# Optimization experiments

Hardware: AMD Instinct MI355X
Metric: run time of the kernel (lower is better)

## Reference

```python
import jax, jax.numpy as jnp
import numpy as np

B, T, D = 2, 2048, 1024
H, HD = 16, 64  # num_heads, num_hiddens_per_head


def setup_inputs() -> dict:
    key = jax.random.key(0)
    ks = jax.random.split(key, 6)
    scale = 1.0 / np.sqrt(D)
    inputs_q = jax.random.normal(ks[0], (B, T, D), dtype=jnp.float32)
    inputs_kv = jax.random.normal(ks[1], (B, T, D), dtype=jnp.float32)
    # causal mask, broadcastable to [b, h, t, T]
    mask = jnp.tril(jnp.ones((T, T), dtype=bool))[None, None, :, :]
    Wq = jax.random.normal(ks[2], (D, H * HD), dtype=jnp.float32) * scale
    Wk = jax.random.normal(ks[3], (D, H * HD), dtype=jnp.float32) * scale
    Wv = jax.random.normal(ks[4], (D, H * HD), dtype=jnp.float32) * scale
    Wo = jax.random.normal(ks[5], (H * HD, D), dtype=jnp.float32) * scale
    return {"inputs_q": inputs_q, "inputs_kv": inputs_kv, "mask": mask,
            "Wq": Wq, "Wk": Wk, "Wv": Wv, "Wo": Wo}


def reference(inputs_q, inputs_kv, mask, Wq, Wk, Wv, Wo):
    b, t, _ = inputs_q.shape
    q = (inputs_q @ Wq).reshape(b, -1, H, HD)
    k = (inputs_kv @ Wk).reshape(b, -1, H, HD)
    v = (inputs_kv @ Wv).reshape(b, -1, H, HD)
    scores = jnp.einsum('bthd,bThd->bhtT', q, k) * (1.0 / jnp.sqrt(HD))
    scores = jnp.where(mask, scores, jnp.finfo(jnp.float32).min)
    attn = jax.nn.softmax(scores, axis=-1)
    out = jnp.einsum('bhtT,bThd->bthd', attn, v).reshape(b, t, H * HD)
    return out @ Wo
```

## Files before the change

kernel.cpp:

```cpp
#include <hip/hip_runtime.h>
#include <hip/hip_bf16.h>

#define B_  2
#define T_  2048
#define D_  1024
#define H_  16
#define HD_ 64

typedef __bf16 bf16x8 __attribute__((ext_vector_type(8)));
typedef float  f32x4  __attribute__((ext_vector_type(4)));

#define MFIX 8.0f

__device__ __forceinline__ __bf16 f2b(float f) {
  __hip_bfloat16 h = __float2bfloat16(f);
  return *reinterpret_cast<__bf16*>(&h);
}

__device__ __forceinline__ void gload_lds16(const __bf16* g, __bf16* l) {
  __builtin_amdgcn_global_load_lds((const unsigned int*)g, (unsigned int*)l, 16, 0, 0);
}

__global__ __launch_bounds__(256) void prep_k(const float* __restrict__ Xq,
                                              const float* __restrict__ Xkv,
                                              const float* __restrict__ Wq,
                                              const float* __restrict__ Wk,
                                              const float* __restrict__ Wv,
                                              const float* __restrict__ Wo,
                                              __hip_bfloat16* __restrict__ Xq_b,
                                              __hip_bfloat16* __restrict__ Xkv_b,
                                              __hip_bfloat16* __restrict__ WTall,
                                              __hip_bfloat16* __restrict__ WoT) {
  const int blk = blockIdx.x;
  if (blk < 8192) {
    const float* x = (blk < 4096) ? Xq : Xkv;
    __hip_bfloat16* y = (blk < 4096) ? Xq_b : Xkv_b;
    const size_t i = ((size_t)(blk & 4095) * 256 + threadIdx.x) * 4;
    f32x4 v = *(const f32x4*)(x + i);
    union { ushort4 u; __hip_bfloat16 h[4]; } o;
#pragma unroll
    for (int j = 0; j < 4; ++j) o.h[j] = __float2bfloat16(v[j]);
    *(ushort4*)(y + i) = o.u;
    return;
  }
  __shared__ float tile[64][65];
  const int wid  = (blk - 8192) >> 8;
  const int tid_ = (blk - 8192) & 255;
  const float* in = (wid == 0) ? Wq : (wid == 1) ? Wk : (wid == 2) ? Wv : Wo;
  __hip_bfloat16* out = (wid == 3) ? WoT : (WTall + (size_t)wid * 1024 * D_);
  const int bx = (tid_ & 15) * 64, by = (tid_ >> 4) * 64;
  const int tx = threadIdx.x & 63, ty = threadIdx.x >> 6;
#pragma unroll
  for (int i = ty; i < 64; i += 4)
    tile[i][tx] = in[(size_t)(by + i) * D_ + bx + tx];
  __syncthreads();
#pragma unroll
  for (int i = ty; i < 64; i += 4)
    out[(size_t)(bx + i) * D_ + by + tx] = __float2bfloat16(tile[tx][i]);
}

__global__ __launch_bounds__(256) void gemm_qkv_k(const __bf16* __restrict__ Aq,
                                                  const __bf16* __restrict__ Akv,
                                                  const __bf16* __restrict__ WTall,
                                                  __hip_bfloat16* __restrict__ Qd,
                                                  __hip_bfloat16* __restrict__ Kd,
                                                  __hip_bfloat16* __restrict__ Vd) {
  __shared__ __align__(16) __bf16 Al[128 * 32];
  __shared__ __align__(16) __bf16 Bl[128 * 32];
  __shared__ __align__(16) __bf16 Tr[64][136];

  const int bm = blockIdx.x * 128;
  const int bn = blockIdx.y * 128;
  const int w  = bn >> 10;
  const __bf16* A = (w == 0) ? Aq : Akv;

  const int wave = threadIdx.x >> 6, lane = threadIdx.x & 63;
  const int wm = (wave >> 1) * 64, wn = (wave & 1) * 64;
  const int lo = lane & 15, qh = lane >> 4;

  const int srow = threadIdx.x >> 2;
  const int skc  = (threadIdx.x & 3) * 8;
  const __bf16* Ag0 = A      + (size_t)(bm + srow) * D_ + skc;
  const __bf16* Bg0 = WTall  + (size_t)(bn + srow) * D_ + skc;
  __bf16* Al0 = Al + threadIdx.x * 8;
  __bf16* Bl0 = Bl + threadIdx.x * 8;

  f32x4 acc[4][4] = {};

  for (int k0 = 0; k0 < D_; k0 += 32) {
    __syncthreads();
    gload_lds16(Ag0 + k0,           Al0);
    gload_lds16(Ag0 + 64 * D_ + k0, Al0 + 64 * 32);
    gload_lds16(Bg0 + k0,           Bl0);
    gload_lds16(Bg0 + 64 * D_ + k0, Bl0 + 64 * 32);
    __syncthreads();

    bf16x8 af[4], bfr[4];
#pragma unroll
    for (int mt = 0; mt < 4; ++mt)
      af[mt] = *(const bf16x8*)(Al + (wm + mt * 16 + lo) * 32 + qh * 8);
#pragma unroll
    for (int nt = 0; nt < 4; ++nt)
      bfr[nt] = *(const bf16x8*)(Bl + (wn + nt * 16 + lo) * 32 + qh * 8);
#pragma unroll
    for (int mt = 0; mt < 4; ++mt)
#pragma unroll
      for (int nt = 0; nt < 4; ++nt)
        acc[mt][nt] = __builtin_amdgcn_mfma_f32_16x16x32_bf16(af[mt], bfr[nt], acc[mt][nt], 0, 0, 0);
  }

  if (w == 2) {
    const int bV  = bm >> 11;
    const int tV0 = bm & (T_ - 1);
#pragma unroll
    for (int ph = 0; ph < 2; ++ph) {
      __syncthreads();
      if ((wn >> 6) == ph) {
#pragma unroll
        for (int mt = 0; mt < 4; ++mt)
#pragma unroll
          for (int nt = 0; nt < 4; ++nt)
#pragma unroll
            for (int r = 0; r < 4; ++r)
              Tr[nt * 16 + lo][wm + mt * 16 + 4 * qh + r] = f2b(acc[mt][nt][r]);
      }
      __syncthreads();
      const int hcol = ((bn & 1023) >> 6) + ph;
      const int row  = threadIdx.x >> 2;
      const int tc   = (threadIdx.x & 3) * 32;
      __hip_bfloat16* dst = Vd + (((size_t)(bV * H_ + hcol) * HD_ + row) * T_) + tV0 + tc;
#pragma unroll
      for (int j = 0; j < 32; j += 8)
        *(bf16x8*)(__bf16*)(dst + j) = *(const bf16x8*)&Tr[row][tc + j];
    }
  } else {
    __hip_bfloat16* dst = (w == 0) ? Qd : Kd;
    const float scale = (w == 0) ? 0.125f : 1.0f;
    const int col0 = (bn + wn) & 1023;
#pragma unroll
    for (int mt = 0; mt < 4; ++mt)
#pragma unroll
      for (int nt = 0; nt < 4; ++nt)
#pragma unroll
        for (int r = 0; r < 4; ++r) {
          const int m = bm + wm + mt * 16 + 4 * qh + r;
          const int n = col0 + nt * 16 + lo;
          const int b = m >> 11, t = m & (T_ - 1);
          const int h = n >> 6,  d = n & 63;
          dst[(((size_t)(b * H_ + h) * T_ + t) << 6) + d] =
              __float2bfloat16(acc[mt][nt][r] * scale);
        }
  }
}

__global__ __launch_bounds__(256) void gemm_out_k(const __bf16* __restrict__ A,
                                                  const __bf16* __restrict__ Bt,
                                                  float* __restrict__ C) {
  __shared__ __align__(16) __bf16 Al[128 * 32];
  __shared__ __align__(16) __bf16 Bl[64 * 32];

  const int bm = blockIdx.x * 128;
  const int bn = blockIdx.y * 64;
  const int wave = threadIdx.x >> 6, lane = threadIdx.x & 63;
  const int wm = (wave >> 1) * 64, wn = (wave & 1) * 32;
  const int lo = lane & 15, qh = lane >> 4;

  const int srow = threadIdx.x >> 2;
  const int skc  = (threadIdx.x & 3) * 8;
  const __bf16* Ag0 = A  + (size_t)(bm + srow) * D_ + skc;
  const __bf16* Bg0 = Bt + (size_t)(bn + srow) * D_ + skc;
  __bf16* Al0 = Al + threadIdx.x * 8;
  __bf16* Bl0 = Bl + threadIdx.x * 8;

  f32x4 acc[4][2] = {};

  for (int k0 = 0; k0 < D_; k0 += 32) {
    __syncthreads();
    gload_lds16(Ag0 + k0,           Al0);
    gload_lds16(Ag0 + 64 * D_ + k0, Al0 + 64 * 32);
    gload_lds16(Bg0 + k0,           Bl0);
    __syncthreads();

    bf16x8 af[4], bfr[2];
#pragma unroll
    for (int mt = 0; mt < 4; ++mt)
      af[mt] = *(const bf16x8*)(Al + (wm + mt * 16 + lo) * 32 + qh * 8);
#pragma unroll
    for (int nt = 0; nt < 2; ++nt)
      bfr[nt] = *(const bf16x8*)(Bl + (wn + nt * 16 + lo) * 32 + qh * 8);
#pragma unroll
    for (int mt = 0; mt < 4; ++mt)
#pragma unroll
      for (int nt = 0; nt < 2; ++nt)
        acc[mt][nt] = __builtin_amdgcn_mfma_f32_16x16x32_bf16(af[mt], bfr[nt], acc[mt][nt], 0, 0, 0);
  }

#pragma unroll
  for (int mt = 0; mt < 4; ++mt)
#pragma unroll
    for (int nt = 0; nt < 2; ++nt)
#pragma unroll
      for (int r = 0; r < 4; ++r) {
        const int m = bm + wm + mt * 16 + 4 * qh + r;
        const int n = bn + wn + nt * 16 + lo;
        C[(size_t)m * D_ + n] = acc[mt][nt][r];
      }
}

__global__ __launch_bounds__(256) void attn_slice_k(const __hip_bfloat16* __restrict__ Q,
                                                    const __hip_bfloat16* __restrict__ K,
                                                    const __hip_bfloat16* __restrict__ Vt,
                                                    __hip_bfloat16* __restrict__ Po,
                                                    float* __restrict__ Lp,
                                                    __hip_bfloat16* __restrict__ AO) {
  __shared__ __align__(16) __bf16 Kl[64 * 64];
  __shared__ __align__(16) __bf16 Vl[64 * 64];
  __shared__ __align__(16) __bf16 Pl[4][16][72];

  const int bh = blockIdx.x;
  const int u  = blockIdx.y;
  int qb, sl;
  if (u < 8)       { qb = u;                    sl = 0; }
  else if (u < 24) { qb = 8  + ((u - 8) >> 1);  sl = (u - 8) & 1; }
  else if (u < 48) { qb = 16 + (u - 24) / 3;    sl = (u - 24) % 3; }
  else             { qb = 24 + ((u - 48) >> 2); sl = (u - 48) & 3; }
  const int jt0 = sl * 8;
  const int jt_end = (jt0 + 8 < qb + 1) ? jt0 + 8 : qb + 1;
  const int t0 = qb * 64;

  const int wave = threadIdx.x >> 6, lane = threadIdx.x & 63;
  const int lo = lane & 15, qh = lane >> 4;

  const __hip_bfloat16* Qb = Q  + (size_t)bh * T_ * HD_;
  const __bf16* Kb = (const __bf16*)(K  + (size_t)bh * T_ * HD_);
  const __bf16* Vb = (const __bf16*)(Vt + (size_t)bh * HD_ * T_);

  const int srow = threadIdx.x >> 3;
  const int ssc  = (threadIdx.x & 7) ^ (srow & 7);
  __bf16* Kd0 = Kl + threadIdx.x * 8;
  __bf16* Kd1 = Kl + 2048 + threadIdx.x * 8;
  __bf16* Vd0 = Vl + threadIdx.x * 8;
  __bf16* Vd1 = Vl + 2048 + threadIdx.x * 8;

  bf16x8 qf[2];
  qf[0] = *(const bf16x8*)(Qb + (size_t)(t0 + wave * 16 + lo) * HD_ + qh * 8);
  qf[1] = *(const bf16x8*)(Qb + (size_t)(t0 + wave * 16 + lo) * HD_ + 32 + qh * 8);

  const int rc0 = (qh)     ^ (lo & 7);
  const int rc1 = (4 + qh) ^ (lo & 7);

  f32x4 o[4] = {};
  float lp[4] = {0.f, 0.f, 0.f, 0.f};

  for (int jt = jt0; jt < jt_end; ++jt) {
    const int jb = jt * 64;
    const bool diag = (jt == qb);

    __syncthreads();
    gload_lds16(Kb + (size_t)(jb + srow)      * HD_ + ssc * 8, Kd0);
    gload_lds16(Kb + (size_t)(jb + 32 + srow) * HD_ + ssc * 8, Kd1);
    gload_lds16(Vb + (size_t)srow        * T_ + jb + ssc * 8, Vd0);
    gload_lds16(Vb + (size_t)(32 + srow) * T_ + jb + ssc * 8, Vd1);
    __syncthreads();

    f32x4 s[4];
#pragma unroll
    for (int nt = 0; nt < 4; ++nt) {
      if (diag && nt > wave) { s[nt] = (f32x4){-1e30f, -1e30f, -1e30f, -1e30f}; continue; }
      f32x4 acc = {0.f, 0.f, 0.f, 0.f};
      bf16x8 kf0 = *(const bf16x8*)(Kl + (nt * 16 + lo) * 64 + rc0 * 8);
      acc = __builtin_amdgcn_mfma_f32_16x16x32_bf16(qf[0], kf0, acc, 0, 0, 0);
      bf16x8 kf1 = *(const bf16x8*)(Kl + (nt * 16 + lo) * 64 + rc1 * 8);
      acc = __builtin_amdgcn_mfma_f32_16x16x32_bf16(qf[1], kf1, acc, 0, 0, 0);
      if (diag && nt == wave) {
#pragma unroll
        for (int r = 0; r < 4; ++r)
          if (lo > 4 * qh + r) acc[r] = -1e30f;
      }
      s[nt] = acc;
    }

#pragma unroll
    for (int nt = 0; nt < 4; ++nt)
#pragma unroll
      for (int r = 0; r < 4; ++r) {
        const float p = __expf(s[nt][r] - MFIX);
        lp[r] += p;
        Pl[wave][4 * qh + r][nt * 16 + lo] = f2b(p);
      }

#pragma unroll
    for (int ks = 0; ks < 2; ++ks) {
      bf16x8 pf = *(const bf16x8*)&Pl[wave][lo][ks * 32 + qh * 8];
      const int rc = ks ? rc1 : rc0;
#pragma unroll
      for (int nt = 0; nt < 4; ++nt) {
        bf16x8 vf = *(const bf16x8*)(Vl + (nt * 16 + lo) * 64 + rc * 8);
        o[nt] = __builtin_amdgcn_mfma_f32_16x16x32_bf16(pf, vf, o[nt], 0, 0, 0);
      }
    }
  }

#pragma unroll
  for (int r = 0; r < 4; ++r)
#pragma unroll
    for (int msk = 1; msk < 16; msk <<= 1)
      lp[r] += __shfl_xor(lp[r], msk, 64);

  if (u < 8) {
    const int b = bh >> 4, h = bh & 15;
#pragma unroll
    for (int nt = 0; nt < 4; ++nt)
#pragma unroll
      for (int r = 0; r < 4; ++r) {
        const int q = t0 + wave * 16 + 4 * qh + r;
        AO[((size_t)(b * T_ + q) << 10) + h * 64 + nt * 16 + lo] =
            __float2bfloat16(o[nt][r] / lp[r]);
      }
  } else {
    __hip_bfloat16* base = Po + (size_t)(bh * 80 + u) * 4096 + (size_t)wave * 16 * 64;
#pragma unroll
    for (int nt = 0; nt < 4; ++nt)
#pragma unroll
      for (int r = 0; r < 4; ++r)
        base[(4 * qh + r) * 64 + nt * 16 + lo] = __float2bfloat16(o[nt][r]);
    if (lo == 0) {
#pragma unroll
      for (int r = 0; r < 4; ++r)
        Lp[(size_t)(bh * 80 + u) * 64 + wave * 16 + 4 * qh + r] = lp[r];
    }
  }
}

__global__ __launch_bounds__(256) void attn_combine_k(const __hip_bfloat16* __restrict__ Po,
                                                      const float* __restrict__ Lp,
                                                      __hip_bfloat16* __restrict__ O) {
  const int bh = blockIdx.x, qb = 8 + blockIdx.y;
  const int ns = (qb >> 3) + 1;
  const int ubase = (qb < 16) ? 8 + 2 * (qb - 8)
                  : (qb < 24) ? 24 + 3 * (qb - 16)
                  : 48 + 4 * (qb - 24);
  const int d = threadIdx.x & 63, r0 = threadIdx.x >> 6;
  const int b = bh >> 4, h = bh & 15;
  const __hip_bfloat16* ub = Po + (size_t)(bh * 80 + ubase) * 4096;
  const float* lb = Lp + (size_t)(bh * 80 + ubase) * 64;

  for (int row = r0; row < 64; row += 4) {
    float acc = 0.f, l = 0.f;
    for (int s = 0; s < ns; ++s) {
      acc += __bfloat162float(ub[(size_t)s * 4096 + row * 64 + d]);
      l   += lb[(size_t)s * 64 + row];
    }
    const int t = qb * 64 + row;
    O[((size_t)(b * T_ + t) << 10) + h * 64 + d] = __float2bfloat16(acc / l);
  }
}

extern "C" void kernel_launch(void* const* d_in, const int* in_sizes, int n_in,
                              void* d_out, int out_size, void* d_ws, size_t ws_size,
                              hipStream_t stream) {
  const float* Xq  = (const float*)d_in[0];
  const float* Xkv = (const float*)d_in[1];
  const float* Wq  = (const float*)d_in[3];
  const float* Wk  = (const float*)d_in[4];
  const float* Wv  = (const float*)d_in[5];
  const float* Wo  = (const float*)d_in[6];

  char* ws = (char*)d_ws;
  const size_t MB = 1024ull * 1024ull;
  __hip_bfloat16* WTall = (__hip_bfloat16*)(ws + 0 * MB);
  __hip_bfloat16* WoT   = (__hip_bfloat16*)(ws + 6 * MB);
  __hip_bfloat16* Qw    = (__hip_bfloat16*)(ws + 8 * MB);
  __hip_bfloat16* Kw    = (__hip_bfloat16*)(ws + 16 * MB);
  __hip_bfloat16* Vw    = (__hip_bfloat16*)(ws + 24 * MB);
  __hip_bfloat16* AO    = (__hip_bfloat16*)(ws + 32 * MB);
  __hip_bfloat16* Po    = (__hip_bfloat16*)(ws + 40 * MB);
  float*          Lpart = (float*)        (ws + 62 * MB);
  __hip_bfloat16* Xq_b  = (__hip_bfloat16*)(ws + 84 * MB);
  __hip_bfloat16* Xkv_b = (__hip_bfloat16*)(ws + 92 * MB);

  const dim3 tb(256);

  prep_k<<<dim3(9216), tb, 0, stream>>>(Xq, Xkv, Wq, Wk, Wv, Wo,
                                        Xq_b, Xkv_b, WTall, WoT);

  gemm_qkv_k<<<dim3(32, 24), tb, 0, stream>>>((const __bf16*)Xq_b, (const __bf16*)Xkv_b,
                                              (const __bf16*)WTall, Qw, Kw, Vw);

  attn_slice_k<<<dim3(B_ * H_, 80), tb, 0, stream>>>(Qw, Kw, Vw, Po, Lpart, AO);
  attn_combine_k<<<dim3(B_ * H_, 24), tb, 0, stream>>>(Po, Lpart, AO);

  gemm_out_k<<<dim3(32, 16), tb, 0, stream>>>((const __bf16*)AO, (const __bf16*)WoT,
                                              (float*)d_out);
}
```

Measured before the change: 227.4 us.

## Enlarge attention query tile to 256 rows with double-buffered K/V staging

Each attention block now handles 256 query rows (64 per wave) instead of 64, so every K/V tile loaded into LDS is reused by four times as many queries, and the split-KV grid shrinks from 80 to 20 slices per head. K/V tiles are double-buffered so the next tile's global-to-LDS load overlaps compute, and the P staging buffer is XOR-swizzled. The softmax scale is folded into Q as a log2(e)/8 factor so the kernel can use exp2 directly with an adjusted fixed max. Register pressure rises (16 output accumulators per wave), and the coarser tiles cut parallelism, with more causal imbalance per block.

Result: slower. 281.5 us (+23.8%).

```diff
diff --git a/kernel.cpp b/kernel.cpp
--- a/kernel.cpp
+++ b/kernel.cpp
@@ -10,7 +10,8 @@
 typedef __bf16 bf16x8 __attribute__((ext_vector_type(8)));
 typedef float  f32x4  __attribute__((ext_vector_type(4)));
 
-#define MFIX 8.0f
+#define MFIX2  11.5415603f
+#define QSCALE 0.18033688f
 
 __device__ __forceinline__ __bf16 f2b(float f) {
   __hip_bfloat16 h = __float2bfloat16(f);
@@ -135,7 +136,7 @@
     }
   } else {
     __hip_bfloat16* dst = (w == 0) ? Qd : Kd;
-    const float scale = (w == 0) ? 0.125f : 1.0f;
+    const float scale = (w == 0) ? QSCALE : 1.0f;
     const int col0 = (bn + wn) & 1023;
 #pragma unroll
     for (int mt = 0; mt < 4; ++mt)
@@ -207,127 +208,162 @@
       }
 }
 
-__global__ __launch_bounds__(256) void attn_slice_k(const __hip_bfloat16* __restrict__ Q,
-                                                    const __hip_bfloat16* __restrict__ K,
-                                                    const __hip_bfloat16* __restrict__ Vt,
-                                                    __hip_bfloat16* __restrict__ Po,
-                                                    float* __restrict__ Lp,
-                                                    __hip_bfloat16* __restrict__ AO) {
-  __shared__ __align__(16) __bf16 Kl[64 * 64];
-  __shared__ __align__(16) __bf16 Vl[64 * 64];
-  __shared__ __align__(16) __bf16 Pl[4][16][72];
+__global__ __launch_bounds__(256, 2) void attn_slice_k(const __hip_bfloat16* __restrict__ Q,
+                                                       const __hip_bfloat16* __restrict__ K,
+                                                       const __hip_bfloat16* __restrict__ Vt,
+                                                       __hip_bfloat16* __restrict__ Po,
+                                                       float* __restrict__ Lp,
+                                                       __hip_bfloat16* __restrict__ AO) {
+  __shared__ __align__(16) __bf16 Kl[2][64 * 64];
+  __shared__ __align__(16) __bf16 Vl[2][64 * 64];
+  __shared__ __align__(16) __bf16 Pl[4][64][64];
 
   const int bh = blockIdx.x;
   const int u  = blockIdx.y;
-  int qb, sl;
-  if (u < 8)       { qb = u;                    sl = 0; }
-  else if (u < 24) { qb = 8  + ((u - 8) >> 1);  sl = (u - 8) & 1; }
-  else if (u < 48) { qb = 16 + (u - 24) / 3;    sl = (u - 24) % 3; }
-  else             { qb = 24 + ((u - 48) >> 2); sl = (u - 48) & 3; }
+  int qi, sl;
+  if (u < 2)       { qi = u;                   sl = 0; }
+  else if (u < 6)  { qi = 2 + ((u - 2) >> 1);  sl = (u - 2) & 1; }
+  else if (u < 12) { qi = 4 + (u - 6) / 3;     sl = (u - 6) % 3; }
+  else             { qi = 6 + ((u - 12) >> 2); sl = (u - 12) & 3; }
+  const int n_i = 4 * qi + 4;
   const int jt0 = sl * 8;
-  const int jt_end = (jt0 + 8 < qb + 1) ? jt0 + 8 : qb + 1;
-  const int t0 = qb * 64;
+  const int jt_end = (jt0 + 8 < n_i) ? jt0 + 8 : n_i;
+  const int t0 = qi * 256;
 
   const int wave = threadIdx.x >> 6, lane = threadIdx.x & 63;
   const int lo = lane & 15, qh = lane >> 4;
-
-  const __hip_bfloat16* Qb = Q  + (size_t)bh * T_ * HD_;
+  const int qw0 = t0 + wave * 64;
+  const int wlast = 4 * qi + wave;
+
+  const __hip_bfloat16* Qb = Q + (size_t)bh * T_ * HD_;
   const __bf16* Kb = (const __bf16*)(K  + (size_t)bh * T_ * HD_);
   const __bf16* Vb = (const __bf16*)(Vt + (size_t)bh * HD_ * T_);
 
   const int srow = threadIdx.x >> 3;
   const int ssc  = (threadIdx.x & 7) ^ (srow & 7);
-  __bf16* Kd0 = Kl + threadIdx.x * 8;
-  __bf16* Kd1 = Kl + 2048 + threadIdx.x * 8;
-  __bf16* Vd0 = Vl + threadIdx.x * 8;
-  __bf16* Vd1 = Vl + 2048 + threadIdx.x * 8;
-
-  bf16x8 qf[2];
-  qf[0] = *(const bf16x8*)(Qb + (size_t)(t0 + wave * 16 + lo) * HD_ + qh * 8);
-  qf[1] = *(const bf16x8*)(Qb + (size_t)(t0 + wave * 16 + lo) * HD_ + 32 + qh * 8);
-
-  const int rc0 = (qh)     ^ (lo & 7);
+
+#define STAGE(buf, jb2)                                                                     \
+  do {                                                                                      \
+    gload_lds16(Kb + (size_t)((jb2) + srow) * HD_ + ssc * 8,      Kl[(buf)] + threadIdx.x * 8);        \
+    gload_lds16(Kb + (size_t)((jb2) + 32 + srow) * HD_ + ssc * 8, Kl[(buf)] + 2048 + threadIdx.x * 8); \
+    gload_lds16(Vb + (size_t)srow * T_ + (jb2) + ssc * 8,         Vl[(buf)] + threadIdx.x * 8);        \
+    gload_lds16(Vb + (size_t)(32 + srow) * T_ + (jb2) + ssc * 8,  Vl[(buf)] + 2048 + threadIdx.x * 8); \
+  } while (0)
+
+  bf16x8 qf[4][2];
+#pragma unroll
+  for (int mt = 0; mt < 4; ++mt)
+#pragma unroll
+    for (int ks = 0; ks < 2; ++ks)
+      qf[mt][ks] = *(const bf16x8*)(Qb + (size_t)(qw0 + mt * 16 + lo) * HD_ + ks * 32 + qh * 8);
+
+  const int rc0 = qh ^ (lo & 7);
   const int rc1 = (4 + qh) ^ (lo & 7);
 
-  f32x4 o[4] = {};
-  float lp[4] = {0.f, 0.f, 0.f, 0.f};
+  f32x4 o[4][4] = {};
+  float lp[16] = {};
+
+  STAGE(0, jt0 * 64);
+  __syncthreads();
+  int cur = 0;
 
   for (int jt = jt0; jt < jt_end; ++jt) {
     const int jb = jt * 64;
-    const bool diag = (jt == qb);
-
+    if (jt + 1 < jt_end) STAGE(cur ^ 1, jb + 64);
+
+    if (jt <= wlast) {
+      bf16x8 kf[4][2];
+#pragma unroll
+      for (int nt = 0; nt < 4; ++nt) {
+        kf[nt][0] = *(const bf16x8*)(Kl[cur] + (nt * 16 + lo) * 64 + rc0 * 8);
+        kf[nt][1] = *(const bf16x8*)(Kl[cur] + (nt * 16 + lo) * 64 + rc1 * 8);
+      }
+#pragma unroll
+      for (int mt = 0; mt < 4; ++mt) {
+        const int qrb = qw0 + mt * 16;
+        if (jb > qrb + 15) continue;
+        f32x4 s[4];
+#pragma unroll
+        for (int nt = 0; nt < 4; ++nt) {
+          const int j0 = jb + nt * 16;
+          if (j0 > qrb + 15) { s[nt] = (f32x4){-1e30f, -1e30f, -1e30f, -1e30f}; continue; }
+          f32x4 acc = {0.f, 0.f, 0.f, 0.f};
+          acc = __builtin_amdgcn_mfma_f32_16x16x32_bf16(qf[mt][0], kf[nt][0], acc, 0, 0, 0);
+          acc = __builtin_amdgcn_mfma_f32_16x16x32_bf16(qf[mt][1], kf[nt][1], acc, 0, 0, 0);
+          if (j0 + 15 > qrb) {
+#pragma unroll
+            for (int r = 0; r < 4; ++r)
+              if (j0 + lo > qrb + 4 * qh + r) acc[r] = -1e30f;
+          }
+          s[nt] = acc;
+        }
+#pragma unroll
+        for (int nt = 0; nt < 4; ++nt)
+#pragma unroll
+          for (int r = 0; r < 4; ++r) {
+            const float p = __builtin_amdgcn_exp2f(s[nt][r] - MFIX2);
+            lp[mt * 4 + r] += p;
+            Pl[wave][mt * 16 + 4 * qh + r]
+              [(((2 * nt) + (lo >> 3)) ^ ((4 * qh + r) & 7)) * 8 + (lo & 7)] = f2b(p);
+          }
+      }
+      bf16x8 vf[2][4];
+#pragma unroll
+      for (int nt = 0; nt < 4; ++nt) {
+        vf[0][nt] = *(const bf16x8*)(Vl[cur] + (nt * 16 + lo) * 64 + rc0 * 8);
+        vf[1][nt] = *(const bf16x8*)(Vl[cur] + (nt * 16 + lo) * 64 + rc1 * 8);
+      }
+#pragma unroll
+      for (int mt = 0; mt < 4; ++mt) {
+        if (jb > qw0 + mt * 16 + 15) continue;
+        bf16x8 pf0 = *(const bf16x8*)&Pl[wave][mt * 16 + lo][rc0 * 8];
+        bf16x8 pf1 = *(const bf16x8*)&Pl[wave][mt * 16 + lo][rc1 * 8];
+#pragma unroll
+        for (int nt = 0; nt < 4; ++nt) {
+          o[mt][nt] = __builtin_amdgcn_mfma_f32_16x16x32_bf16(pf0, vf[0][nt], o[mt][nt], 0, 0, 0);
+          o[mt][nt] = __builtin_amdgcn_mfma_f32_16x16x32_bf16(pf1, vf[1][nt], o[mt][nt], 0, 0, 0);
+        }
+      }
+    }
     __syncthreads();
-    gload_lds16(Kb + (size_t)(jb + srow)      * HD_ + ssc * 8, Kd0);
-    gload_lds16(Kb + (size_t)(jb + 32 + srow) * HD_ + ssc * 8, Kd1);
-    gload_lds16(Vb + (size_t)srow        * T_ + jb + ssc * 8, Vd0);
-    gload_lds16(Vb + (size_t)(32 + srow) * T_ + jb + ssc * 8, Vd1);
-    __syncthreads();
-
-    f32x4 s[4];
-#pragma unroll
-    for (int nt = 0; nt < 4; ++nt) {
-      if (diag && nt > wave) { s[nt] = (f32x4){-1e30f, -1e30f, -1e30f, -1e30f}; continue; }
-      f32x4 acc = {0.f, 0.f, 0.f, 0.f};
-      bf16x8 kf0 = *(const bf16x8*)(Kl + (nt * 16 + lo) * 64 + rc0 * 8);
-      acc = __builtin_amdgcn_mfma_f32_16x16x32_bf16(qf[0], kf0, acc, 0, 0, 0);
-      bf16x8 kf1 = *(const bf16x8*)(Kl + (nt * 16 + lo) * 64 + rc1 * 8);
-      acc = __builtin_amdgcn_mfma_f32_16x16x32_bf16(qf[1], kf1, acc, 0, 0, 0);
-      if (diag && nt == wave) {
+    cur ^= 1;
+  }
+#undef STAGE
+
+#pragma unroll
+  for (int i = 0; i < 16; ++i)
+#pragma unroll
+    for (int msk = 1; msk < 16; msk <<= 1)
+      lp[i] += __shfl_xor(lp[i], msk, 64);
+
+  if (u < 2) {
+    const int b = bh >> 4, h = bh & 15;
+#pragma unroll
+    for (int mt = 0; mt < 4; ++mt)
+#pragma unroll
+      for (int nt = 0; nt < 4; ++nt)
+#pragma unroll
+        for (int r = 0; r < 4; ++r) {
+          const int q = qw0 + mt * 16 + 4 * qh + r;
+          AO[((size_t)(b * T_ + q) << 10) + h * 64 + nt * 16 + lo] =
+              __float2bfloat16(o[mt][nt][r] / lp[mt * 4 + r]);
+        }
+  } else {
+    __hip_bfloat16* base = Po + ((size_t)(bh * 20 + u) * 256 + wave * 64) * 64;
+#pragma unroll
+    for (int mt = 0; mt < 4; ++mt)
+#pragma unroll
+      for (int nt = 0; nt < 4; ++nt)
 #pragma unroll
         for (int r = 0; r < 4; ++r)
-          if (lo > 4 * qh + r) acc[r] = -1e30f;
-      }
-      s[nt] = acc;
-    }
-
-#pragma unroll
-    for (int nt = 0; nt < 4; ++nt)
-#pragma unroll
-      for (int r = 0; r < 4; ++r) {
-        const float p = __expf(s[nt][r] - MFIX);
-        lp[r] += p;
-        Pl[wave][4 * qh + r][nt * 16 + lo] = f2b(p);
-      }
-
-#pragma unroll
-    for (int ks = 0; ks < 2; ++ks) {
-      bf16x8 pf = *(const bf16x8*)&Pl[wave][lo][ks * 32 + qh * 8];
-      const int rc = ks ? rc1 : rc0;
-#pragma unroll
-      for (int nt = 0; nt < 4; ++nt) {
-        bf16x8 vf = *(const bf16x8*)(Vl + (nt * 16 + lo) * 64 + rc * 8);
-        o[nt] = __builtin_amdgcn_mfma_f32_16x16x32_bf16(pf, vf, o[nt], 0, 0, 0);
-      }
-    }
-  }
-
-#pragma unroll
-  for (int r = 0; r < 4; ++r)
-#pragma unroll
-    for (int msk = 1; msk < 16; msk <<= 1)
-      lp[r] += __shfl_xor(lp[r], msk, 64);
-
-  if (u < 8) {
-    const int b = bh >> 4, h = bh & 15;
-#pragma unroll
-    for (int nt = 0; nt < 4; ++nt)
-#pragma unroll
-      for (int r = 0; r < 4; ++r) {
-        const int q = t0 + wave * 16 + 4 * qh + r;
-        AO[((size_t)(b * T_ + q) << 10) + h * 64 + nt * 16 + lo] =
-            __float2bfloat16(o[nt][r] / lp[r]);
-      }
-  } else {
-    __hip_bfloat16* base = Po + (size_t)(bh * 80 + u) * 4096 + (size_t)wave * 16 * 64;
-#pragma unroll
-    for (int nt = 0; nt < 4; ++nt)
-#pragma unroll
-      for (int r = 0; r < 4; ++r)
-        base[(4 * qh + r) * 64 + nt * 16 + lo] = __float2bfloat16(o[nt][r]);
+          base[(mt * 16 + 4 * qh + r) * 64 + nt * 16 + lo] = __float2bfloat16(o[mt][nt][r]);
     if (lo == 0) {
-#pragma unroll
-      for (int r = 0; r < 4; ++r)
-        Lp[(size_t)(bh * 80 + u) * 64 + wave * 16 + 4 * qh + r] = lp[r];
+      float* lpb = Lp + (size_t)(bh * 20 + u) * 256 + wave * 64;
+#pragma unroll
+      for (int mt = 0; mt < 4; ++mt)
+#pragma unroll
+        for (int r = 0; r < 4; ++r)
+          lpb[mt * 16 + 4 * qh + r] = lp[mt * 4 + r];
     }
   }
 }
@@ -335,23 +371,24 @@
 __global__ __launch_bounds__(256) void attn_combine_k(const __hip_bfloat16* __restrict__ Po,
                                                       const float* __restrict__ Lp,
                                                       __hip_bfloat16* __restrict__ O) {
-  const int bh = blockIdx.x, qb = 8 + blockIdx.y;
-  const int ns = (qb >> 3) + 1;
-  const int ubase = (qb < 16) ? 8 + 2 * (qb - 8)
-                  : (qb < 24) ? 24 + 3 * (qb - 16)
-                  : 48 + 4 * (qb - 24);
+  const int bh = blockIdx.x;
+  const int qi = 2 + blockIdx.y;
+  const int ns = (qi >> 1) + 1;
+  const int ubase = (qi < 4) ? 2 + 2 * (qi - 2)
+                  : (qi < 6) ? 6 + 3 * (qi - 4)
+                  : 12 + 4 * (qi - 6);
   const int d = threadIdx.x & 63, r0 = threadIdx.x >> 6;
   const int b = bh >> 4, h = bh & 15;
-  const __hip_bfloat16* ub = Po + (size_t)(bh * 80 + ubase) * 4096;
-  const float* lb = Lp + (size_t)(bh * 80 + ubase) * 64;
-
-  for (int row = r0; row < 64; row += 4) {
+  const __hip_bfloat16* ub = Po + (size_t)(bh * 20 + ubase) * 16384;
+  const float* lb = Lp + (size_t)(bh * 20 + ubase) * 256;
+
+  for (int row = r0; row < 256; row += 4) {
     float acc = 0.f, l = 0.f;
     for (int s = 0; s < ns; ++s) {
-      acc += __bfloat162float(ub[(size_t)s * 4096 + row * 64 + d]);
-      l   += lb[(size_t)s * 64 + row];
+      acc += __bfloat162float(ub[(size_t)s * 16384 + row * 64 + d]);
+      l   += lb[(size_t)s * 256 + row];
     }
-    const int t = qb * 64 + row;
+    const int t = qi * 256 + row;
     O[((size_t)(b * T_ + t) << 10) + h * 64 + d] = __float2bfloat16(acc / l);
   }
 }
@@ -387,8 +424,8 @@
   gemm_qkv_k<<<dim3(32, 24), tb, 0, stream>>>((const __bf16*)Xq_b, (const __bf16*)Xkv_b,
                                               (const __bf16*)WTall, Qw, Kw, Vw);
 
-  attn_slice_k<<<dim3(B_ * H_, 80), tb, 0, stream>>>(Qw, Kw, Vw, Po, Lpart, AO);
-  attn_combine_k<<<dim3(B_ * H_, 24), tb, 0, stream>>>(Po, Lpart, AO);
+  attn_slice_k<<<dim3(B_ * H_, 20), tb, 0, stream>>>(Qw, Kw, Vw, Po, Lpart, AO);
+  attn_combine_k<<<dim3(B_ * H_, 6), tb, 0, stream>>>(Po, Lpart, AO);
 
   gemm_out_k<<<dim3(32, 16), tb, 0, stream>>>((const __bf16*)AO, (const __bf16*)WoT,
                                               (float*)d_out);
```
